# Kernel optimization log

Measured on AMD Instinct MI355X. Metric: run time of the kernel, lower is better.

The kernel has to match this reference:

```python
import jax, jax.numpy as jnp
import numpy as np

DIM = 64
NUM_HEADS = 2
SR = 2


def _conv(x, w, stride):
    # x: [B,C,H,W], w: [O,I,kh,kw], no bias (qkv_bias=False)
    return jax.lax.conv_general_dilated(
        x, w, window_strides=(stride, stride), padding='VALID',
        dimension_numbers=('NCHW', 'OIHW', 'NCHW'))


def setup_inputs() -> dict:
    key = jax.random.key(0)
    kx, kq, kk, kv, kp = jax.random.split(key, 5)
    x = jax.random.normal(kx, (16, DIM, 64, 64), dtype=jnp.float32)
    s = 0.05
    wq = jax.random.normal(kq, (DIM, DIM, 1, 1), dtype=jnp.float32) * s
    wk = jax.random.normal(kk, (DIM, DIM, SR, SR), dtype=jnp.float32) * s
    wv = jax.random.normal(kv, (DIM, DIM, SR, SR), dtype=jnp.float32) * s
    wproj = jax.random.normal(kp, (DIM, DIM, 1, 1), dtype=jnp.float32) * s
    return {'x': x, 'wq': wq, 'wk': wk, 'wv': wv, 'wproj': wproj}


def reference(x, wq, wk, wv, wproj):
    B, C, H, W = x.shape
    h = NUM_HEADS
    hd = C // h
    scale = hd ** (-0.5)
    # Q: 1x1 conv, keeps spatial size; K/V: sr x sr conv with stride sr
    q = _conv(x, wq, 1).reshape(B, h, hd, -1)        # [B,h,hd,N]
    k = _conv(x, wk, SR).reshape(B, h, hd, -1)       # [B,h,hd,Nkv]
    v = _conv(x, wv, SR).reshape(B, h, hd, -1)       # [B,h,hd,Nkv]
    # attn = q^T @ k * scale -> [B,h,N,Nkv]
    attn = jnp.einsum('bhdn,bhdm->bhnm', q, k) * scale
    attn = jax.nn.softmax(attn, axis=-1)
    # out = v @ attn^T -> [B,h,hd,N]
    out = jnp.einsum('bhdm,bhnm->bhdn', v, attn)
    out = out.reshape(B, C, H, W)
    return _conv(out, wproj, 1)
```

## Files before the change

kernel.cpp:

```cpp
#include <hip/hip_runtime.h>
#include <hip/hip_bf16.h>


#define B_ 16
#define C_ 64
#define N_ 4096
#define NKV_ 1024

typedef __bf16 bf16x8 __attribute__((ext_vector_type(8)));
typedef __bf16 bf16x4 __attribute__((ext_vector_type(4)));
typedef float f32x4 __attribute__((ext_vector_type(4)));

__global__ __launch_bounds__(256) void conv1x1_k(const float* __restrict__ X,
                                                 const float* __restrict__ W,
                                                 float* __restrict__ Y) {
    __shared__ float xs[64][132];
    __shared__ float ws[64][65];
    const int b = blockIdx.x;
    const int n0 = blockIdx.y * 128;
    const int t = threadIdx.x;

    for (int idx = t; idx < 64 * 64; idx += 256) ws[idx >> 6][idx & 63] = W[idx];
    const float* Xb = X + (size_t)b * C_ * N_ + n0;
    for (int idx = t; idx < 64 * 128; idx += 256) {
        int ci = idx >> 7, n = idx & 127;
        xs[ci][n] = Xb[ci * N_ + n];
    }
    __syncthreads();

    const int co0 = (t >> 4) * 4;
    const int nn0 = (t & 15) * 8;
    float acc[4][8];
#pragma unroll
    for (int k = 0; k < 4; ++k)
#pragma unroll
        for (int j = 0; j < 8; ++j) acc[k][j] = 0.f;

    for (int ci = 0; ci < 64; ++ci) {
        float w0 = ws[co0 + 0][ci], w1 = ws[co0 + 1][ci];
        float w2 = ws[co0 + 2][ci], w3 = ws[co0 + 3][ci];
        float4 xa = *(const float4*)&xs[ci][nn0];
        float4 xb = *(const float4*)&xs[ci][nn0 + 4];
        float xv[8] = {xa.x, xa.y, xa.z, xa.w, xb.x, xb.y, xb.z, xb.w};
#pragma unroll
        for (int j = 0; j < 8; ++j) {
            acc[0][j] = fmaf(w0, xv[j], acc[0][j]);
            acc[1][j] = fmaf(w1, xv[j], acc[1][j]);
            acc[2][j] = fmaf(w2, xv[j], acc[2][j]);
            acc[3][j] = fmaf(w3, xv[j], acc[3][j]);
        }
    }
    float* Yb = Y + (size_t)b * C_ * N_ + n0;
#pragma unroll
    for (int k = 0; k < 4; ++k) {
        float4 o0 = {acc[k][0], acc[k][1], acc[k][2], acc[k][3]};
        float4 o1 = {acc[k][4], acc[k][5], acc[k][6], acc[k][7]};
        *(float4*)&Yb[(co0 + k) * N_ + nn0] = o0;
        *(float4*)&Yb[(co0 + k) * N_ + nn0 + 4] = o1;
    }
}

__global__ __launch_bounds__(256) void qconv_k(const float* __restrict__ X,
                                               const float* __restrict__ W,
                                               __bf16* __restrict__ Qt) {
    __shared__ float xs[64][132];
    __shared__ float ws[64][65];
    const int b = blockIdx.x;
    const int n0 = blockIdx.y * 128;
    const int t = threadIdx.x;
    const float scale = 0.25503487572f;

    for (int idx = t; idx < 64 * 64; idx += 256) ws[idx >> 6][idx & 63] = W[idx];
    const float* Xb = X + (size_t)b * C_ * N_ + n0;
    for (int idx = t; idx < 64 * 128; idx += 256) {
        int ci = idx >> 7, n = idx & 127;
        xs[ci][n] = Xb[ci * N_ + n];
    }
    __syncthreads();

    const int co0 = (t & 15) * 4;
    const int nn0 = (t >> 4) * 8;
    float acc[4][8];
#pragma unroll
    for (int k = 0; k < 4; ++k)
#pragma unroll
        for (int j = 0; j < 8; ++j) acc[k][j] = 0.f;

    for (int ci = 0; ci < 64; ++ci) {
        float w0 = ws[co0 + 0][ci], w1 = ws[co0 + 1][ci];
        float w2 = ws[co0 + 2][ci], w3 = ws[co0 + 3][ci];
        float4 xa = *(const float4*)&xs[ci][nn0];
        float4 xb = *(const float4*)&xs[ci][nn0 + 4];
        float xv[8] = {xa.x, xa.y, xa.z, xa.w, xb.x, xb.y, xb.z, xb.w};
#pragma unroll
        for (int j = 0; j < 8; ++j) {
            acc[0][j] = fmaf(w0, xv[j], acc[0][j]);
            acc[1][j] = fmaf(w1, xv[j], acc[1][j]);
            acc[2][j] = fmaf(w2, xv[j], acc[2][j]);
            acc[3][j] = fmaf(w3, xv[j], acc[3][j]);
        }
    }
    const int h = co0 >> 5, d0 = co0 & 31;
    __bf16* Qb = Qt + (size_t)(b * 2 + h) * N_ * 32;
#pragma unroll
    for (int j = 0; j < 8; ++j) {
        bf16x4 v = {(__bf16)(acc[0][j] * scale), (__bf16)(acc[1][j] * scale),
                    (__bf16)(acc[2][j] * scale), (__bf16)(acc[3][j] * scale)};
        *(bf16x4*)&Qb[(size_t)(n0 + nn0 + j) * 32 + d0] = v;
    }
}

__global__ __launch_bounds__(256) void convkv_k(const float* __restrict__ X,
                                                const float* __restrict__ Wk,
                                                const float* __restrict__ Wv,
                                                __bf16* __restrict__ Kt,
                                                __bf16* __restrict__ Vh) {
    __shared__ float xs[64][64];
    __shared__ float ws[64][65];
    const int b = blockIdx.x;
    const int m0 = blockIdx.y * 64;
    const int kv = blockIdx.z;
    const int i0 = m0 >> 5;
    const int t = threadIdx.x;
    const int co0 = kv ? (t >> 4) * 4 : (t & 15) * 4;
    const int mm0 = kv ? (t & 15) * 4 : (t >> 4) * 4;
    const float* Wsel = kv ? Wv : Wk;

    float acc[4][4];
#pragma unroll
    for (int k = 0; k < 4; ++k)
#pragma unroll
        for (int m = 0; m < 4; ++m) acc[k][m] = 0.f;

    const float* Xb = X + (size_t)b * C_ * N_;

    for (int ch = 0; ch < 4; ++ch) {
        for (int idx = t; idx < 4096; idx += 256) {
            int co = idx >> 6, rl = idx & 63;
            ws[co][rl] = Wsel[co * 256 + ch * 64 + rl];
        }
        for (int idx = t; idx < 4096; idx += 256) {
            int rl = idx >> 6, ml = idx & 63;
            int ci = ch * 16 + (rl >> 2);
            int di = (rl >> 1) & 1, dj = rl & 1;
            int i = i0 + (ml >> 5), j = ml & 31;
            xs[rl][ml] = Xb[ci * N_ + (2 * i + di) * 64 + (2 * j + dj)];
        }
        __syncthreads();
        for (int rl = 0; rl < 64; ++rl) {
            float4 xv4 = *(const float4*)&xs[rl][mm0];
            float xa[4] = {xv4.x, xv4.y, xv4.z, xv4.w};
#pragma unroll
            for (int k = 0; k < 4; ++k) {
                float wv = ws[co0 + k][rl];
#pragma unroll
                for (int m = 0; m < 4; ++m) acc[k][m] = fmaf(wv, xa[m], acc[k][m]);
            }
        }
        __syncthreads();
    }
    const int h = co0 >> 5, d0 = co0 & 31;
    if (kv) {
        __bf16* Vb = Vh + (size_t)(b * 2 + h) * 32 * NKV_;
#pragma unroll
        for (int k = 0; k < 4; ++k) {
            bf16x4 vv = {(__bf16)acc[k][0], (__bf16)acc[k][1],
                         (__bf16)acc[k][2], (__bf16)acc[k][3]};
            *(bf16x4*)&Vb[(size_t)(d0 + k) * NKV_ + m0 + mm0] = vv;
        }
    } else {
        __bf16* Kb = Kt + (size_t)(b * 2 + h) * NKV_ * 32;
#pragma unroll
        for (int mq = 0; mq < 4; ++mq) {
            bf16x4 kvv = {(__bf16)acc[0][mq], (__bf16)acc[1][mq],
                          (__bf16)acc[2][mq], (__bf16)acc[3][mq]};
            *(bf16x4*)&Kb[(size_t)(m0 + mm0 + mq) * 32 + d0] = kvv;
        }
    }
}

__global__ __launch_bounds__(256, 4) void attn_mfma(const __bf16* __restrict__ Qt,
                                                    const __bf16* __restrict__ Kt,
                                                    const __bf16* __restrict__ Vh,
                                                    float* __restrict__ O) {
    __shared__ __attribute__((aligned(16))) __bf16 Pls[4][2][16][40];
    const int bh = blockIdx.x;
    const int w = threadIdx.x >> 6;
    const int l = threadIdx.x & 63;
    const int lr = l & 15, lg = l >> 4;
    const int nb = blockIdx.y * 128 + w * 32;

    const __bf16* Qb = Qt + (size_t)bh * N_ * 32;
    const __bf16* Kb = Kt + (size_t)bh * NKV_ * 32;
    const __bf16* Vb = Vh + (size_t)bh * 32 * NKV_;

    bf16x8 qf0 = *(const bf16x8*)&Qb[(size_t)(nb + lr) * 32 + 8 * lg];
    bf16x8 qf1 = *(const bf16x8*)&Qb[(size_t)(nb + 16 + lr) * 32 + 8 * lg];
    const __bf16* Krow = Kb + (size_t)lr * 32 + 8 * lg;
    const __bf16* V0 = Vb + (size_t)lr * NKV_ + 8 * lg;
    const __bf16* V1 = Vb + (size_t)(16 + lr) * NKV_ + 8 * lg;

    f32x4 oacc00 = {0,0,0,0}, oacc01 = {0,0,0,0}, oacc10 = {0,0,0,0}, oacc11 = {0,0,0,0};
    float lsum0 = 0.f, lsum1 = 0.f;

    bf16x8 kf0 = *(const bf16x8*)&Krow[0];
    bf16x8 kf1 = *(const bf16x8*)&Krow[16 * 32];
    bf16x8 vf0 = *(const bf16x8*)&V0[0];
    bf16x8 vf1 = *(const bf16x8*)&V1[0];

    for (int mb = 0; mb < NKV_; mb += 32) {
        const int mn = (mb + 32) & (NKV_ - 1);
        bf16x8 nk0 = *(const bf16x8*)&Krow[(size_t)mn * 32];
        bf16x8 nk1 = *(const bf16x8*)&Krow[(size_t)(mn + 16) * 32];
        bf16x8 nv0 = *(const bf16x8*)&V0[mn];
        bf16x8 nv1 = *(const bf16x8*)&V1[mn];

        __builtin_amdgcn_s_setprio(1);
        f32x4 s00 = __builtin_amdgcn_mfma_f32_16x16x32_bf16(kf0, qf0, (f32x4){0,0,0,0}, 0, 0, 0);
        f32x4 s10 = __builtin_amdgcn_mfma_f32_16x16x32_bf16(kf1, qf0, (f32x4){0,0,0,0}, 0, 0, 0);
        f32x4 s01 = __builtin_amdgcn_mfma_f32_16x16x32_bf16(kf0, qf1, (f32x4){0,0,0,0}, 0, 0, 0);
        f32x4 s11 = __builtin_amdgcn_mfma_f32_16x16x32_bf16(kf1, qf1, (f32x4){0,0,0,0}, 0, 0, 0);
        __builtin_amdgcn_s_setprio(0);

        float p00[4], p10[4], p01[4], p11[4];
#pragma unroll
        for (int r = 0; r < 4; ++r) {
            p00[r] = __builtin_amdgcn_exp2f(s00[r]);
            p10[r] = __builtin_amdgcn_exp2f(s10[r]);
            p01[r] = __builtin_amdgcn_exp2f(s01[r]);
            p11[r] = __builtin_amdgcn_exp2f(s11[r]);
        }
        lsum0 += ((p00[0] + p00[1]) + (p00[2] + p00[3])) + ((p10[0] + p10[1]) + (p10[2] + p10[3]));
        lsum1 += ((p01[0] + p01[1]) + (p01[2] + p01[3])) + ((p11[0] + p11[1]) + (p11[2] + p11[3]));

        bf16x4 w00 = {(__bf16)p00[0], (__bf16)p00[1], (__bf16)p00[2], (__bf16)p00[3]};
        bf16x4 w10 = {(__bf16)p10[0], (__bf16)p10[1], (__bf16)p10[2], (__bf16)p10[3]};
        bf16x4 w01 = {(__bf16)p01[0], (__bf16)p01[1], (__bf16)p01[2], (__bf16)p01[3]};
        bf16x4 w11 = {(__bf16)p11[0], (__bf16)p11[1], (__bf16)p11[2], (__bf16)p11[3]};
        *(bf16x4*)&Pls[w][0][lr][4 * lg] = w00;
        *(bf16x4*)&Pls[w][0][lr][16 + 4 * lg] = w10;
        *(bf16x4*)&Pls[w][1][lr][4 * lg] = w01;
        *(bf16x4*)&Pls[w][1][lr][16 + 4 * lg] = w11;

        bf16x8 af0 = *(const bf16x8*)&Pls[w][0][lr][8 * lg];
        bf16x8 af1 = *(const bf16x8*)&Pls[w][1][lr][8 * lg];

        __builtin_amdgcn_s_setprio(1);
        oacc00 = __builtin_amdgcn_mfma_f32_16x16x32_bf16(af0, vf0, oacc00, 0, 0, 0);
        oacc01 = __builtin_amdgcn_mfma_f32_16x16x32_bf16(af0, vf1, oacc01, 0, 0, 0);
        oacc10 = __builtin_amdgcn_mfma_f32_16x16x32_bf16(af1, vf0, oacc10, 0, 0, 0);
        oacc11 = __builtin_amdgcn_mfma_f32_16x16x32_bf16(af1, vf1, oacc11, 0, 0, 0);
        __builtin_amdgcn_s_setprio(0);

        kf0 = nk0; kf1 = nk1; vf0 = nv0; vf1 = nv1;
    }

    lsum0 += __shfl_xor(lsum0, 16, 64);
    lsum0 += __shfl_xor(lsum0, 32, 64);
    lsum1 += __shfl_xor(lsum1, 16, 64);
    lsum1 += __shfl_xor(lsum1, 32, 64);
    float inv0[4], inv1[4];
#pragma unroll
    for (int r = 0; r < 4; ++r) {
        inv0[r] = 1.0f / __shfl(lsum0, 4 * lg + r, 64);
        inv1[r] = 1.0f / __shfl(lsum1, 4 * lg + r, 64);
    }

    const int b = bh >> 1, h = bh & 1;
    const size_t c0 = (size_t)b * 64 + h * 32 + lr;
    float4 o;
    o = (float4){oacc00[0]*inv0[0], oacc00[1]*inv0[1], oacc00[2]*inv0[2], oacc00[3]*inv0[3]};
    *(float4*)&O[c0 * N_ + nb + 4 * lg] = o;
    o = (float4){oacc01[0]*inv0[0], oacc01[1]*inv0[1], oacc01[2]*inv0[2], oacc01[3]*inv0[3]};
    *(float4*)&O[(c0 + 16) * N_ + nb + 4 * lg] = o;
    o = (float4){oacc10[0]*inv1[0], oacc10[1]*inv1[1], oacc10[2]*inv1[2], oacc10[3]*inv1[3]};
    *(float4*)&O[c0 * N_ + nb + 16 + 4 * lg] = o;
    o = (float4){oacc11[0]*inv1[0], oacc11[1]*inv1[1], oacc11[2]*inv1[2], oacc11[3]*inv1[3]};
    *(float4*)&O[(c0 + 16) * N_ + nb + 16 + 4 * lg] = o;
}

extern "C" void kernel_launch(void* const* d_in, const int* in_sizes, int n_in,
                              void* d_out, int out_size, void* d_ws, size_t ws_size,
                              hipStream_t stream) {
    const float* x     = (const float*)d_in[0];
    const float* wq    = (const float*)d_in[1];
    const float* wk    = (const float*)d_in[2];
    const float* wv    = (const float*)d_in[3];
    const float* wproj = (const float*)d_in[4];
    float* out = (float*)d_out;

    char* ws = (char*)d_ws;
    __bf16* Qt = (__bf16*)ws;
    __bf16* Kt = (__bf16*)(ws + 8388608);
    __bf16* Vh = (__bf16*)(ws + 8388608 + 2097152);
    float*  O  = (float*)(ws + 8388608 + 2097152 + 2097152);

    qconv_k <<<dim3(B_, N_ / 128), 256, 0, stream>>>(x, wq, Qt);
    convkv_k<<<dim3(B_, NKV_ / 64, 2), 256, 0, stream>>>(x, wk, wv, Kt, Vh);
    attn_mfma<<<dim3(B_ * 2, N_ / 128), 256, 0, stream>>>(Qt, Kt, Vh, O);
    conv1x1_k<<<dim3(B_, N_ / 128), 256, 0, stream>>>(O, wproj, out);
}
```

Baseline: 177.8 us.

## Move Q/KV/projection convolutions to bf16 MFMA and write attention output as bf16

New measurement: 163.6 us. -8.0%, faster.

```diff
diff --git a/kernel.cpp b/kernel.cpp
--- a/kernel.cpp
+++ b/kernel.cpp
@@ -11,207 +11,156 @@
 typedef __bf16 bf16x4 __attribute__((ext_vector_type(4)));
 typedef float f32x4 __attribute__((ext_vector_type(4)));
 
-__global__ __launch_bounds__(256) void conv1x1_k(const float* __restrict__ X,
-                                                 const float* __restrict__ W,
-                                                 float* __restrict__ Y) {
-    __shared__ float xs[64][132];
-    __shared__ float ws[64][65];
-    const int b = blockIdx.x;
-    const int n0 = blockIdx.y * 128;
-    const int t = threadIdx.x;
-
-    for (int idx = t; idx < 64 * 64; idx += 256) ws[idx >> 6][idx & 63] = W[idx];
+__global__ __launch_bounds__(256) void qconv_mfma(const float* __restrict__ X,
+                                                  const float* __restrict__ W,
+                                                  __bf16* __restrict__ Qt) {
+    __shared__ __bf16 xls[128][72];
+    const int b = blockIdx.x, n0 = blockIdx.y * 128, t = threadIdx.x;
+    const int w = t >> 6, l = t & 63, lr = l & 15, lg = l >> 4;
+    const float scale = 0.25503487572f;
+
     const float* Xb = X + (size_t)b * C_ * N_ + n0;
-    for (int idx = t; idx < 64 * 128; idx += 256) {
-        int ci = idx >> 7, n = idx & 127;
-        xs[ci][n] = Xb[ci * N_ + n];
-    }
+    for (int idx = t; idx < 2048; idx += 256) {
+        int ci = idx >> 5, n4 = (idx & 31) * 4;
+        float4 v = *(const float4*)&Xb[ci * N_ + n4];
+        xls[n4 + 0][ci] = (__bf16)v.x; xls[n4 + 1][ci] = (__bf16)v.y;
+        xls[n4 + 2][ci] = (__bf16)v.z; xls[n4 + 3][ci] = (__bf16)v.w;
+    }
+    bf16x8 a[4][2];
+#pragma unroll
+    for (int cot = 0; cot < 4; ++cot)
+#pragma unroll
+        for (int ks = 0; ks < 2; ++ks) {
+            const float* wp = &W[(cot * 16 + lr) * 64 + ks * 32 + 8 * lg];
+            float4 w0 = *(const float4*)wp;
+            float4 w1 = *(const float4*)(wp + 4);
+            a[cot][ks] = (bf16x8){(__bf16)(w0.x * scale), (__bf16)(w0.y * scale),
+                                  (__bf16)(w0.z * scale), (__bf16)(w0.w * scale),
+                                  (__bf16)(w1.x * scale), (__bf16)(w1.y * scale),
+                                  (__bf16)(w1.z * scale), (__bf16)(w1.w * scale)};
+        }
     __syncthreads();
 
-    const int co0 = (t >> 4) * 4;
-    const int nn0 = (t & 15) * 8;
-    float acc[4][8];
-#pragma unroll
-    for (int k = 0; k < 4; ++k)
-#pragma unroll
-        for (int j = 0; j < 8; ++j) acc[k][j] = 0.f;
-
-    for (int ci = 0; ci < 64; ++ci) {
-        float w0 = ws[co0 + 0][ci], w1 = ws[co0 + 1][ci];
-        float w2 = ws[co0 + 2][ci], w3 = ws[co0 + 3][ci];
-        float4 xa = *(const float4*)&xs[ci][nn0];
-        float4 xb = *(const float4*)&xs[ci][nn0 + 4];
-        float xv[8] = {xa.x, xa.y, xa.z, xa.w, xb.x, xb.y, xb.z, xb.w};
-#pragma unroll
-        for (int j = 0; j < 8; ++j) {
-            acc[0][j] = fmaf(w0, xv[j], acc[0][j]);
-            acc[1][j] = fmaf(w1, xv[j], acc[1][j]);
-            acc[2][j] = fmaf(w2, xv[j], acc[2][j]);
-            acc[3][j] = fmaf(w3, xv[j], acc[3][j]);
-        }
-    }
-    float* Yb = Y + (size_t)b * C_ * N_ + n0;
-#pragma unroll
-    for (int k = 0; k < 4; ++k) {
-        float4 o0 = {acc[k][0], acc[k][1], acc[k][2], acc[k][3]};
-        float4 o1 = {acc[k][4], acc[k][5], acc[k][6], acc[k][7]};
-        *(float4*)&Yb[(co0 + k) * N_ + nn0] = o0;
-        *(float4*)&Yb[(co0 + k) * N_ + nn0 + 4] = o1;
-    }
-}
-
-__global__ __launch_bounds__(256) void qconv_k(const float* __restrict__ X,
-                                               const float* __restrict__ W,
-                                               __bf16* __restrict__ Qt) {
-    __shared__ float xs[64][132];
-    __shared__ float ws[64][65];
-    const int b = blockIdx.x;
-    const int n0 = blockIdx.y * 128;
-    const int t = threadIdx.x;
-    const float scale = 0.25503487572f;
-
-    for (int idx = t; idx < 64 * 64; idx += 256) ws[idx >> 6][idx & 63] = W[idx];
-    const float* Xb = X + (size_t)b * C_ * N_ + n0;
-    for (int idx = t; idx < 64 * 128; idx += 256) {
-        int ci = idx >> 7, n = idx & 127;
-        xs[ci][n] = Xb[ci * N_ + n];
+#pragma unroll
+    for (int ns = 0; ns < 2; ++ns) {
+        const int nloc = w * 32 + ns * 16 + lr;
+        bf16x8 bb0 = *(const bf16x8*)&xls[nloc][8 * lg];
+        bf16x8 bb1 = *(const bf16x8*)&xls[nloc][32 + 8 * lg];
+        f32x4 acc[4];
+#pragma unroll
+        for (int cot = 0; cot < 4; ++cot) acc[cot] = (f32x4){0.f, 0.f, 0.f, 0.f};
+#pragma unroll
+        for (int cot = 0; cot < 4; ++cot) {
+            acc[cot] = __builtin_amdgcn_mfma_f32_16x16x32_bf16(a[cot][0], bb0, acc[cot], 0, 0, 0);
+            acc[cot] = __builtin_amdgcn_mfma_f32_16x16x32_bf16(a[cot][1], bb1, acc[cot], 0, 0, 0);
+        }
+        __bf16* qp = Qt + (size_t)b * N_ * 64 + (size_t)(n0 + nloc) * 64;
+#pragma unroll
+        for (int cot = 0; cot < 4; ++cot) {
+            bf16x4 ov = {(__bf16)acc[cot][0], (__bf16)acc[cot][1],
+                         (__bf16)acc[cot][2], (__bf16)acc[cot][3]};
+            *(bf16x4*)&qp[cot * 16 + 4 * lg] = ov;
+        }
+    }
+}
+
+__global__ __launch_bounds__(256) void kvconv_mfma(const float* __restrict__ X,
+                                                   const float* __restrict__ Wk,
+                                                   const float* __restrict__ Wv,
+                                                   __bf16* __restrict__ Kt,
+                                                   __bf16* __restrict__ Vh) {
+    __shared__ __bf16 xls[4][2][32][72];
+    __shared__ __bf16 Ws[4][64][72];
+    const int b = blockIdx.x, m0 = blockIdx.y * 64, kv = blockIdx.z;
+    const int i0 = m0 >> 5;
+    const int t = threadIdx.x, w = t >> 6, l = t & 63, lr = l & 15, lg = l >> 4;
+    const float* Wsel = kv ? Wv : Wk;
+
+    for (int idx = t; idx < 16384; idx += 256) {
+        int co = idx >> 8, rem = idx & 255, ci = rem >> 2, tap = rem & 3;
+        Ws[tap][co][ci] = (__bf16)Wsel[idx];
+    }
+    const float* Xb = X + (size_t)b * C_ * N_;
+    for (int idx = t; idx < 4096; idx += 256) {
+        int ci = idx >> 6, rem = idx & 63, p = rem >> 4, c4 = (rem & 15) * 4;
+        float4 v = *(const float4*)&Xb[ci * N_ + (2 * i0 + p) * 64 + c4];
+        xls[p][0][(c4 >> 1) + 0][ci] = (__bf16)v.x;
+        xls[p][1][(c4 >> 1) + 0][ci] = (__bf16)v.y;
+        xls[p][0][(c4 >> 1) + 1][ci] = (__bf16)v.z;
+        xls[p][1][(c4 >> 1) + 1][ci] = (__bf16)v.w;
     }
     __syncthreads();
 
-    const int co0 = (t & 15) * 4;
-    const int nn0 = (t >> 4) * 8;
-    float acc[4][8];
-#pragma unroll
-    for (int k = 0; k < 4; ++k)
-#pragma unroll
-        for (int j = 0; j < 8; ++j) acc[k][j] = 0.f;
-
-    for (int ci = 0; ci < 64; ++ci) {
-        float w0 = ws[co0 + 0][ci], w1 = ws[co0 + 1][ci];
-        float w2 = ws[co0 + 2][ci], w3 = ws[co0 + 3][ci];
-        float4 xa = *(const float4*)&xs[ci][nn0];
-        float4 xb = *(const float4*)&xs[ci][nn0 + 4];
-        float xv[8] = {xa.x, xa.y, xa.z, xa.w, xb.x, xb.y, xb.z, xb.w};
-#pragma unroll
-        for (int j = 0; j < 8; ++j) {
-            acc[0][j] = fmaf(w0, xv[j], acc[0][j]);
-            acc[1][j] = fmaf(w1, xv[j], acc[1][j]);
-            acc[2][j] = fmaf(w2, xv[j], acc[2][j]);
-            acc[3][j] = fmaf(w3, xv[j], acc[3][j]);
-        }
-    }
-    const int h = co0 >> 5, d0 = co0 & 31;
-    __bf16* Qb = Qt + (size_t)(b * 2 + h) * N_ * 32;
-#pragma unroll
-    for (int j = 0; j < 8; ++j) {
-        bf16x4 v = {(__bf16)(acc[0][j] * scale), (__bf16)(acc[1][j] * scale),
-                    (__bf16)(acc[2][j] * scale), (__bf16)(acc[3][j] * scale)};
-        *(bf16x4*)&Qb[(size_t)(n0 + nn0 + j) * 32 + d0] = v;
-    }
-}
-
-__global__ __launch_bounds__(256) void convkv_k(const float* __restrict__ X,
-                                                const float* __restrict__ Wk,
-                                                const float* __restrict__ Wv,
-                                                __bf16* __restrict__ Kt,
-                                                __bf16* __restrict__ Vh) {
-    __shared__ float xs[64][64];
-    __shared__ float ws[64][65];
-    const int b = blockIdx.x;
-    const int m0 = blockIdx.y * 64;
-    const int kv = blockIdx.z;
-    const int i0 = m0 >> 5;
-    const int t = threadIdx.x;
-    const int co0 = kv ? (t >> 4) * 4 : (t & 15) * 4;
-    const int mm0 = kv ? (t & 15) * 4 : (t >> 4) * 4;
-    const float* Wsel = kv ? Wv : Wk;
-
-    float acc[4][4];
-#pragma unroll
-    for (int k = 0; k < 4; ++k)
-#pragma unroll
-        for (int m = 0; m < 4; ++m) acc[k][m] = 0.f;
-
-    const float* Xb = X + (size_t)b * C_ * N_;
-
-    for (int ch = 0; ch < 4; ++ch) {
-        for (int idx = t; idx < 4096; idx += 256) {
-            int co = idx >> 6, rl = idx & 63;
-            ws[co][rl] = Wsel[co * 256 + ch * 64 + rl];
-        }
-        for (int idx = t; idx < 4096; idx += 256) {
-            int rl = idx >> 6, ml = idx & 63;
-            int ci = ch * 16 + (rl >> 2);
-            int di = (rl >> 1) & 1, dj = rl & 1;
-            int i = i0 + (ml >> 5), j = ml & 31;
-            xs[rl][ml] = Xb[ci * N_ + (2 * i + di) * 64 + (2 * j + dj)];
-        }
-        __syncthreads();
-        for (int rl = 0; rl < 64; ++rl) {
-            float4 xv4 = *(const float4*)&xs[rl][mm0];
-            float xa[4] = {xv4.x, xv4.y, xv4.z, xv4.w};
-#pragma unroll
-            for (int k = 0; k < 4; ++k) {
-                float wv = ws[co0 + k][rl];
-#pragma unroll
-                for (int m = 0; m < 4; ++m) acc[k][m] = fmaf(wv, xa[m], acc[k][m]);
+    const int iw = w >> 1, jw = (w & 1) * 16;
+    f32x4 acc[4];
+#pragma unroll
+    for (int cot = 0; cot < 4; ++cot) acc[cot] = (f32x4){0.f, 0.f, 0.f, 0.f};
+#pragma unroll
+    for (int tap = 0; tap < 4; ++tap) {
+        const int di = tap >> 1, dj = tap & 1;
+#pragma unroll
+        for (int ks = 0; ks < 2; ++ks) {
+            bf16x8 bb = *(const bf16x8*)&xls[2 * iw + di][dj][jw + lr][ks * 32 + 8 * lg];
+#pragma unroll
+            for (int cot = 0; cot < 4; ++cot) {
+                bf16x8 aa = *(const bf16x8*)&Ws[tap][cot * 16 + lr][ks * 32 + 8 * lg];
+                acc[cot] = __builtin_amdgcn_mfma_f32_16x16x32_bf16(aa, bb, acc[cot], 0, 0, 0);
             }
         }
-        __syncthreads();
-    }
-    const int h = co0 >> 5, d0 = co0 & 31;
-    if (kv) {
-        __bf16* Vb = Vh + (size_t)(b * 2 + h) * 32 * NKV_;
-#pragma unroll
-        for (int k = 0; k < 4; ++k) {
-            bf16x4 vv = {(__bf16)acc[k][0], (__bf16)acc[k][1],
-                         (__bf16)acc[k][2], (__bf16)acc[k][3]};
-            *(bf16x4*)&Vb[(size_t)(d0 + k) * NKV_ + m0 + mm0] = vv;
+    }
+    const int m = m0 + iw * 32 + jw + lr;
+    if (kv == 0) {
+        __bf16* kp = Kt + (size_t)b * NKV_ * 64 + (size_t)m * 64;
+#pragma unroll
+        for (int cot = 0; cot < 4; ++cot) {
+            bf16x4 ov = {(__bf16)acc[cot][0], (__bf16)acc[cot][1],
+                         (__bf16)acc[cot][2], (__bf16)acc[cot][3]};
+            *(bf16x4*)&kp[cot * 16 + 4 * lg] = ov;
         }
     } else {
-        __bf16* Kb = Kt + (size_t)(b * 2 + h) * NKV_ * 32;
-#pragma unroll
-        for (int mq = 0; mq < 4; ++mq) {
-            bf16x4 kvv = {(__bf16)acc[0][mq], (__bf16)acc[1][mq],
-                          (__bf16)acc[2][mq], (__bf16)acc[3][mq]};
-            *(bf16x4*)&Kb[(size_t)(m0 + mm0 + mq) * 32 + d0] = kvv;
-        }
+        __bf16* vp = Vh + (size_t)b * 64 * NKV_;
+#pragma unroll
+        for (int cot = 0; cot < 4; ++cot)
+#pragma unroll
+            for (int r = 0; r < 4; ++r)
+                vp[(size_t)(cot * 16 + 4 * lg + r) * NKV_ + m] = (__bf16)acc[cot][r];
     }
 }
 
 __global__ __launch_bounds__(256, 4) void attn_mfma(const __bf16* __restrict__ Qt,
                                                     const __bf16* __restrict__ Kt,
                                                     const __bf16* __restrict__ Vh,
-                                                    float* __restrict__ O) {
+                                                    __bf16* __restrict__ OT) {
     __shared__ __attribute__((aligned(16))) __bf16 Pls[4][2][16][40];
     const int bh = blockIdx.x;
+    const int b = bh >> 1, h = bh & 1;
     const int w = threadIdx.x >> 6;
     const int l = threadIdx.x & 63;
     const int lr = l & 15, lg = l >> 4;
     const int nb = blockIdx.y * 128 + w * 32;
 
-    const __bf16* Qb = Qt + (size_t)bh * N_ * 32;
-    const __bf16* Kb = Kt + (size_t)bh * NKV_ * 32;
-    const __bf16* Vb = Vh + (size_t)bh * 32 * NKV_;
-
-    bf16x8 qf0 = *(const bf16x8*)&Qb[(size_t)(nb + lr) * 32 + 8 * lg];
-    bf16x8 qf1 = *(const bf16x8*)&Qb[(size_t)(nb + 16 + lr) * 32 + 8 * lg];
-    const __bf16* Krow = Kb + (size_t)lr * 32 + 8 * lg;
-    const __bf16* V0 = Vb + (size_t)lr * NKV_ + 8 * lg;
-    const __bf16* V1 = Vb + (size_t)(16 + lr) * NKV_ + 8 * lg;
+    const __bf16* Qb = Qt + (size_t)b * N_ * 64;
+    const __bf16* Kb = Kt + (size_t)b * NKV_ * 64;
+    const __bf16* Vb = Vh + (size_t)b * 64 * NKV_;
+
+    bf16x8 qf0 = *(const bf16x8*)&Qb[(size_t)(nb + lr) * 64 + h * 32 + 8 * lg];
+    bf16x8 qf1 = *(const bf16x8*)&Qb[(size_t)(nb + 16 + lr) * 64 + h * 32 + 8 * lg];
+    const __bf16* Krow = Kb + (size_t)lr * 64 + h * 32 + 8 * lg;
+    const __bf16* V0 = Vb + (size_t)(h * 32 + lr) * NKV_ + 8 * lg;
+    const __bf16* V1 = V0 + (size_t)16 * NKV_;
 
     f32x4 oacc00 = {0,0,0,0}, oacc01 = {0,0,0,0}, oacc10 = {0,0,0,0}, oacc11 = {0,0,0,0};
     float lsum0 = 0.f, lsum1 = 0.f;
 
     bf16x8 kf0 = *(const bf16x8*)&Krow[0];
-    bf16x8 kf1 = *(const bf16x8*)&Krow[16 * 32];
+    bf16x8 kf1 = *(const bf16x8*)&Krow[(size_t)16 * 64];
     bf16x8 vf0 = *(const bf16x8*)&V0[0];
     bf16x8 vf1 = *(const bf16x8*)&V1[0];
 
     for (int mb = 0; mb < NKV_; mb += 32) {
         const int mn = (mb + 32) & (NKV_ - 1);
-        bf16x8 nk0 = *(const bf16x8*)&Krow[(size_t)mn * 32];
-        bf16x8 nk1 = *(const bf16x8*)&Krow[(size_t)(mn + 16) * 32];
+        bf16x8 nk0 = *(const bf16x8*)&Krow[(size_t)mn * 64];
+        bf16x8 nk1 = *(const bf16x8*)&Krow[(size_t)(mn + 16) * 64];
         bf16x8 nv0 = *(const bf16x8*)&V0[mn];
         bf16x8 nv1 = *(const bf16x8*)&V1[mn];
 
@@ -246,10 +195,10 @@
         bf16x8 af1 = *(const bf16x8*)&Pls[w][1][lr][8 * lg];
 
         __builtin_amdgcn_s_setprio(1);
-        oacc00 = __builtin_amdgcn_mfma_f32_16x16x32_bf16(af0, vf0, oacc00, 0, 0, 0);
-        oacc01 = __builtin_amdgcn_mfma_f32_16x16x32_bf16(af0, vf1, oacc01, 0, 0, 0);
-        oacc10 = __builtin_amdgcn_mfma_f32_16x16x32_bf16(af1, vf0, oacc10, 0, 0, 0);
-        oacc11 = __builtin_amdgcn_mfma_f32_16x16x32_bf16(af1, vf1, oacc11, 0, 0, 0);
+        oacc00 = __builtin_amdgcn_mfma_f32_16x16x32_bf16(vf0, af0, oacc00, 0, 0, 0);
+        oacc01 = __builtin_amdgcn_mfma_f32_16x16x32_bf16(vf1, af0, oacc01, 0, 0, 0);
+        oacc10 = __builtin_amdgcn_mfma_f32_16x16x32_bf16(vf0, af1, oacc10, 0, 0, 0);
+        oacc11 = __builtin_amdgcn_mfma_f32_16x16x32_bf16(vf1, af1, oacc11, 0, 0, 0);
         __builtin_amdgcn_s_setprio(0);
 
         kf0 = nk0; kf1 = nk1; vf0 = nv0; vf1 = nv1;
@@ -259,24 +208,64 @@
     lsum0 += __shfl_xor(lsum0, 32, 64);
     lsum1 += __shfl_xor(lsum1, 16, 64);
     lsum1 += __shfl_xor(lsum1, 32, 64);
-    float inv0[4], inv1[4];
-#pragma unroll
-    for (int r = 0; r < 4; ++r) {
-        inv0[r] = 1.0f / __shfl(lsum0, 4 * lg + r, 64);
-        inv1[r] = 1.0f / __shfl(lsum1, 4 * lg + r, 64);
-    }
-
-    const int b = bh >> 1, h = bh & 1;
-    const size_t c0 = (size_t)b * 64 + h * 32 + lr;
-    float4 o;
-    o = (float4){oacc00[0]*inv0[0], oacc00[1]*inv0[1], oacc00[2]*inv0[2], oacc00[3]*inv0[3]};
-    *(float4*)&O[c0 * N_ + nb + 4 * lg] = o;
-    o = (float4){oacc01[0]*inv0[0], oacc01[1]*inv0[1], oacc01[2]*inv0[2], oacc01[3]*inv0[3]};
-    *(float4*)&O[(c0 + 16) * N_ + nb + 4 * lg] = o;
-    o = (float4){oacc10[0]*inv1[0], oacc10[1]*inv1[1], oacc10[2]*inv1[2], oacc10[3]*inv1[3]};
-    *(float4*)&O[c0 * N_ + nb + 16 + 4 * lg] = o;
-    o = (float4){oacc11[0]*inv1[0], oacc11[1]*inv1[1], oacc11[2]*inv1[2], oacc11[3]*inv1[3]};
-    *(float4*)&O[(c0 + 16) * N_ + nb + 16 + 4 * lg] = o;
+    const float inv0 = 1.0f / lsum0;
+    const float inv1 = 1.0f / lsum1;
+
+    __bf16* ob = OT + (size_t)b * N_ * 64;
+    bf16x4 s;
+    s = (bf16x4){(__bf16)(oacc00[0]*inv0), (__bf16)(oacc00[1]*inv0),
+                 (__bf16)(oacc00[2]*inv0), (__bf16)(oacc00[3]*inv0)};
+    *(bf16x4*)&ob[(size_t)(nb + lr) * 64 + h * 32 + 4 * lg] = s;
+    s = (bf16x4){(__bf16)(oacc01[0]*inv0), (__bf16)(oacc01[1]*inv0),
+                 (__bf16)(oacc01[2]*inv0), (__bf16)(oacc01[3]*inv0)};
+    *(bf16x4*)&ob[(size_t)(nb + lr) * 64 + h * 32 + 16 + 4 * lg] = s;
+    s = (bf16x4){(__bf16)(oacc10[0]*inv1), (__bf16)(oacc10[1]*inv1),
+                 (__bf16)(oacc10[2]*inv1), (__bf16)(oacc10[3]*inv1)};
+    *(bf16x4*)&ob[(size_t)(nb + 16 + lr) * 64 + h * 32 + 4 * lg] = s;
+    s = (bf16x4){(__bf16)(oacc11[0]*inv1), (__bf16)(oacc11[1]*inv1),
+                 (__bf16)(oacc11[2]*inv1), (__bf16)(oacc11[3]*inv1)};
+    *(bf16x4*)&ob[(size_t)(nb + 16 + lr) * 64 + h * 32 + 16 + 4 * lg] = s;
+}
+
+__global__ __launch_bounds__(256) void proj_mfma(const __bf16* __restrict__ OT,
+                                                 const float* __restrict__ W,
+                                                 float* __restrict__ out) {
+    const int b = blockIdx.x, n0 = blockIdx.y * 128, t = threadIdx.x;
+    const int w = t >> 6, l = t & 63, lr = l & 15, lg = l >> 4;
+
+    bf16x8 a[4][2];
+#pragma unroll
+    for (int cot = 0; cot < 4; ++cot)
+#pragma unroll
+        for (int ks = 0; ks < 2; ++ks) {
+            const float* wp = &W[(cot * 16 + lr) * 64 + ks * 32 + 8 * lg];
+            float4 w0 = *(const float4*)wp;
+            float4 w1 = *(const float4*)(wp + 4);
+            a[cot][ks] = (bf16x8){(__bf16)w0.x, (__bf16)w0.y, (__bf16)w0.z, (__bf16)w0.w,
+                                  (__bf16)w1.x, (__bf16)w1.y, (__bf16)w1.z, (__bf16)w1.w};
+        }
+
+#pragma unroll
+    for (int ns = 0; ns < 2; ++ns) {
+        const int n_g = n0 + w * 32 + ns * 16 + lr;
+        const __bf16* op = OT + (size_t)b * N_ * 64 + (size_t)n_g * 64;
+        bf16x8 bb0 = *(const bf16x8*)&op[8 * lg];
+        bf16x8 bb1 = *(const bf16x8*)&op[32 + 8 * lg];
+        f32x4 acc[4];
+#pragma unroll
+        for (int cot = 0; cot < 4; ++cot) acc[cot] = (f32x4){0.f, 0.f, 0.f, 0.f};
+#pragma unroll
+        for (int cot = 0; cot < 4; ++cot) {
+            acc[cot] = __builtin_amdgcn_mfma_f32_16x16x32_bf16(a[cot][0], bb0, acc[cot], 0, 0, 0);
+            acc[cot] = __builtin_amdgcn_mfma_f32_16x16x32_bf16(a[cot][1], bb1, acc[cot], 0, 0, 0);
+        }
+        float* yb = out + (size_t)b * C_ * N_ + n_g;
+#pragma unroll
+        for (int cot = 0; cot < 4; ++cot)
+#pragma unroll
+            for (int r = 0; r < 4; ++r)
+                yb[(size_t)(cot * 16 + 4 * lg + r) * N_] = acc[cot][r];
+    }
 }
 
 extern "C" void kernel_launch(void* const* d_in, const int* in_sizes, int n_in,
@@ -293,10 +282,10 @@
     __bf16* Qt = (__bf16*)ws;
     __bf16* Kt = (__bf16*)(ws + 8388608);
     __bf16* Vh = (__bf16*)(ws + 8388608 + 2097152);
-    float*  O  = (float*)(ws + 8388608 + 2097152 + 2097152);
-
-    qconv_k <<<dim3(B_, N_ / 128), 256, 0, stream>>>(x, wq, Qt);
-    convkv_k<<<dim3(B_, NKV_ / 64, 2), 256, 0, stream>>>(x, wk, wv, Kt, Vh);
-    attn_mfma<<<dim3(B_ * 2, N_ / 128), 256, 0, stream>>>(Qt, Kt, Vh, O);
-    conv1x1_k<<<dim3(B_, N_ / 128), 256, 0, stream>>>(O, wproj, out);
-}
+    __bf16* OT = (__bf16*)(ws + 8388608 + 2097152 + 2097152);
+
+    qconv_mfma <<<dim3(B_, N_ / 128), 256, 0, stream>>>(x, wq, Qt);
+    kvconv_mfma<<<dim3(B_, NKV_ / 64, 2), 256, 0, stream>>>(x, wk, wv, Kt, Vh);
+    attn_mfma  <<<dim3(B_ * 2, N_ / 128), 256, 0, stream>>>(Qt, Kt, Vh, OT);
+    proj_mfma  <<<dim3(B_, N_ / 128), 256, 0, stream>>>(OT, wproj, out);
+}
```
